# Kernel optimization log

Measured on AMD Instinct MI355X. Metric: run time of the kernel, lower is better.

## Reference

```python
import jax, jax.numpy as jnp
import numpy as np
from jax import lax

C = 8          # bargs.channel
S = 1024       # bargs.test_sidelen
SIGMA = 1.0    # edge_sigma
KS = int(6 * SIGMA + 1)   # 7
PAD = KS // 2             # 3
BW = S // 6               # border_width
LAM, MU, TH = 5.0, 5.0, 1e-4


def _edge_kernel():
    coords = jnp.arange(KS, dtype=jnp.float32) - (KS - 1.0) / 2.0
    g1 = jnp.exp(-coords ** 2 / (2.0 * SIGMA ** 2))
    g1 = g1 / g1.sum()
    g2 = jnp.outer(g1, g1)
    return jnp.broadcast_to(g2, (C, 1, KS, KS))  # depthwise OIHW


def _alpha():
    # max applicable loop index among {row-dist, col-dist}; interior stays 1.
    r = jnp.arange(S)
    g = jnp.where(r < BW, r, jnp.where(S - 1 - r < BW, S - 1 - r, -1))  # [S]
    m = jnp.maximum(g[:, None], g[None, :])                              # [S,S]
    a = jnp.where(m >= 0, m.astype(jnp.float32) / BW, 1.0)
    return a[None, None]  # [1,1,S,S] broadcasts over channels


def _grad_spectrum():
    gv = jnp.array([[-1., -2., -1.], [0., 0., 0.], [1., 2., 1.]], jnp.float32)
    gh = gv.T
    gvf = jnp.fft.fft2(gv, s=(S, S))
    ghf = jnp.fft.fft2(gh, s=(S, S))
    return (jnp.abs(gvf) ** 2 + jnp.abs(ghf) ** 2).astype(jnp.float32)  # real


def _edge_blur(img, kernel, alpha):
    blurred = lax.conv_general_dilated(
        img, kernel, window_strides=(1, 1), padding=[(PAD, PAD), (PAD, PAD)],
        feature_group_count=C, dimension_numbers=('NCHW', 'OIHW', 'NCHW'))
    return alpha * img + (1.0 - alpha) * blurred


def setup_inputs() -> dict:
    key = jax.random.key(0)
    k1, k2 = jax.random.split(key)
    lms = jax.random.uniform(k1, (1, C, S, S), dtype=jnp.float32)
    fuse = jax.random.uniform(k2, (1, C, S, S), dtype=jnp.float32)
    return {"lms": lms, "fuse": fuse}


def reference(lms, fuse):
    kernel = _edge_kernel()
    alpha = _alpha()
    grad = _grad_spectrum()

    lms_fft = jnp.fft.fft2(_edge_blur(lms, kernel, alpha))
    fuse_fft = jnp.fft.fft2(_edge_blur(fuse, kernel, alpha))

    denom = jnp.abs(fuse_fft) ** 2 + LAM + MU * grad      # real [1,C,S,S]
    numer = jnp.conj(fuse_fft) * lms_fft
    psf = jnp.fft.fftshift(jnp.real(jnp.fft.ifft2(numer / denom)), axes=(-2, -1))
    psf = jnp.where(psf < TH, 0.0, psf)                   # [1,C,S,S]

    def crop(p):  # p: [S,S]
        row, col = jnp.unravel_index(jnp.argmax(p), p.shape)
        patch = lax.dynamic_slice(p, (row - 20, col - 20), (41, 41))
        return patch / jnp.sum(patch)

    psf_l = jax.vmap(crop)(psf[0])        # [C,41,41]
    return psf_l[:, None]                 # [C,1,41,41]
```

## Files before the change

kernel.cpp:

```cpp
#include <hip/hip_runtime.h>
#include <math.h>

#define SS 1024
#define NC 8
#define BWD 170
#define THRESH 1e-4f

typedef unsigned long long ull;

__device__ __forceinline__ float2 cmul(float2 a, float2 b) {
    return make_float2(a.x * b.x - a.y * b.y, a.x * b.y + a.y * b.x);
}

#define XS(a) ((a) ^ (((a) >> 4) & 15))

template <int DIR>
__device__ __forceinline__ void bfly4(const float2 v[4], float2 r[4]) {
    float2 a = v[0], b = v[1], c = v[2], d = v[3];
    float2 apc = make_float2(a.x + c.x, a.y + c.y);
    float2 amc = make_float2(a.x - c.x, a.y - c.y);
    float2 bpd = make_float2(b.x + d.x, b.y + d.y);
    float2 jb  = make_float2(-(b.y - d.y), b.x - d.x);
    r[0] = make_float2(apc.x + bpd.x, apc.y + bpd.y);
    r[2] = make_float2(apc.x - bpd.x, apc.y - bpd.y);
    if (DIR == -1) {
        r[1] = make_float2(amc.x - jb.x, amc.y - jb.y);
        r[3] = make_float2(amc.x + jb.x, amc.y + jb.y);
    } else {
        r[1] = make_float2(amc.x + jb.x, amc.y + jb.y);
        r[3] = make_float2(amc.x - jb.x, amc.y - jb.y);
    }
}

template <int DIR>
__device__ __forceinline__ void fft1024_reg(float2 v[4], float2* A, float2* B,
                                            int tid) {
    float2* dst = A;
    float2* alt = B;
    #pragma unroll
    for (int t = 0; t < 4; ++t) {
        int s = 1 << (2 * t);
        int k = tid & ~(s - 1);
        float2 r[4];
        bfly4<DIR>(v, r);
        float rev = (float)k * (1.0f / 1024.0f);
        float2 w1 = make_float2(__builtin_amdgcn_cosf(rev),
                                (float)DIR * __builtin_amdgcn_sinf(rev));
        float2 w2 = cmul(w1, w1);
        float2 w3 = cmul(w2, w1);
        int base = tid + 3 * k;
        dst[XS(base)]         = r[0];
        dst[XS(base + s)]     = cmul(r[1], w1);
        dst[XS(base + 2 * s)] = cmul(r[2], w2);
        dst[XS(base + 3 * s)] = cmul(r[3], w3);
        __syncthreads();
        v[0] = dst[XS(tid)];
        v[1] = dst[XS(tid + 256)];
        v[2] = dst[XS(tid + 512)];
        v[3] = dst[XS(tid + 768)];
        float2* tmp = dst; dst = alt; alt = tmp;
    }
    float2 r[4];
    bfly4<DIR>(v, r);
    v[0] = r[0]; v[1] = r[1]; v[2] = r[2]; v[3] = r[3];
}

#define PIDX(r) ((r) + ((r) >> 5))

__global__ __launch_bounds__(256) void blur_fft_kernel(
        const float* __restrict__ lms, const float* __restrict__ fuse,
        float2* __restrict__ Zf) {
    __shared__ float2 bufA[1024];
    __shared__ float2 smemB2[1068];
    float* rowl = (float*)smemB2;
    float* rowf = rowl + 1068;
    int tid = threadIdx.x;
    int g = blockIdx.x;
    int c = g >> 10;
    int y = (g & 7) * 128 + ((g >> 3) & 127);
    const float* L = lms + ((size_t)c << 20);
    const float* F = fuse + ((size_t)c << 20);
    int x0 = tid << 2;

    double e1 = exp(-0.5), e2 = exp(-2.0), e3 = exp(-4.5);
    double sm = 1.0 + 2.0 * (e1 + e2 + e3);
    float w[7] = { (float)(e3 / sm), (float)(e2 / sm), (float)(e1 / sm),
                   (float)(1.0 / sm),
                   (float)(e1 / sm), (float)(e2 / sm), (float)(e3 / sm) };

    bool rowInt = (y >= BWD) && (y <= SS - 1 - BWD);
    bool skipLoads = rowInt && (tid >= 45) && (tid <= 210);
    bool doH = !rowInt || (tid <= 43) || (tid >= 212);

    float4 cl, cf;
    if (skipLoads) {
        cl = *(const float4*)&L[((size_t)y << 10) + x0];
        cf = *(const float4*)&F[((size_t)y << 10) + x0];
    } else {
        float4 lv[7], fv[7];
        #pragma unroll
        for (int r = 0; r < 7; ++r) {
            int gy = y - 3 + r;
            if (gy >= 0 && gy < SS) {
                lv[r] = *(const float4*)&L[((size_t)gy << 10) + x0];
                fv[r] = *(const float4*)&F[((size_t)gy << 10) + x0];
            } else {
                lv[r] = make_float4(0.f, 0.f, 0.f, 0.f);
                fv[r] = make_float4(0.f, 0.f, 0.f, 0.f);
            }
        }
        cl = lv[3]; cf = fv[3];
        #pragma unroll
        for (int j = 0; j < 4; ++j) {
            float a = 0.f, b = 0.f;
            #pragma unroll
            for (int r = 0; r < 7; ++r) {
                a += w[r] * (&lv[r].x)[j];
                b += w[r] * (&fv[r].x)[j];
            }
            rowl[PIDX(3 + x0 + j)] = a;
            rowf[PIDX(3 + x0 + j)] = b;
        }
    }
    if (tid < 3) {
        rowl[PIDX(tid)] = 0.f; rowf[PIDX(tid)] = 0.f;
        rowl[PIDX(1027 + tid)] = 0.f; rowf[PIDX(1027 + tid)] = 0.f;
    }
    __syncthreads();

    float bl[4] = {0.f, 0.f, 0.f, 0.f}, bf[4] = {0.f, 0.f, 0.f, 0.f};
    if (doH) {
        #pragma unroll
        for (int k = 0; k < 4; ++k) {
            float a = 0.f, b = 0.f;
            #pragma unroll
            for (int j = 0; j < 7; ++j) {
                a += w[j] * rowl[PIDX(x0 + k + j)];
                b += w[j] * rowf[PIDX(x0 + k + j)];
            }
            bl[k] = a; bf[k] = b;
        }
    }
    int gyv = (y < BWD) ? y : ((SS - 1 - y) < BWD ? (SS - 1 - y) : -1);
    #pragma unroll
    for (int k = 0; k < 4; ++k) {
        int x = x0 + k;
        int gx = (x < BWD) ? x : ((SS - 1 - x) < BWD ? (SS - 1 - x) : -1);
        int m = gyv > gx ? gyv : gx;
        float a = (m >= 0) ? (float)m / (float)BWD : 1.0f;
        bufA[XS(x)] = make_float2(a * (&cl.x)[k] + (1.0f - a) * bl[k],
                                  a * (&cf.x)[k] + (1.0f - a) * bf[k]);
    }
    __syncthreads();

    float2 v[4];
    #pragma unroll
    for (int m = 0; m < 4; ++m) v[m] = bufA[XS(tid + (m << 8))];
    fft1024_reg<-1>(v, smemB2, bufA, tid);

    float2* Zrow = Zf + (((size_t)c << 20) + ((size_t)y << 10));
    #pragma unroll
    for (int r = 0; r < 4; ++r) Zrow[tid + (r << 8)] = v[r];
}

__global__ __launch_bounds__(256) void fft2_wiener_kernel(
        const float2* __restrict__ Z, float2* __restrict__ Wb) {
    __shared__ float2 resbuf[4][1024];
    __shared__ float2 scratch[1024];
    int tid = threadIdx.x;
    int p = blockIdx.x >> 9;
    int i0 = blockIdx.x & 511;
    int i = ((i0 & 7) << 3) | ((i0 >> 3) & 7) | (i0 & ~63);
    int rows[2];
    rows[0] = (i == 0) ? 0 : i;
    rows[1] = (i == 0) ? 512 : 1024 - i;
    bool selfp = (i == 0);

    float2 v[4], nv[4];
    {
        const float2* g0 = Z + (((size_t)(2 * p) << 20) + rows[0]);
        #pragma unroll
        for (int m = 0; m < 4; ++m)
            v[m] = g0[(size_t)(tid + (m << 8)) << 10];
    }
    #pragma unroll
    for (int combo = 0; combo < 4; ++combo) {
        if (combo < 3) {
            int nr = (combo + 1) >> 1, nc = (combo + 1) & 1;
            const float2* gn = Z + (((size_t)(2 * p + nc) << 20) + rows[nr]);
            #pragma unroll
            for (int m = 0; m < 4; ++m)
                nv[m] = gn[(size_t)(tid + (m << 8)) << 10];
        }
        fft1024_reg<-1>(v, scratch, resbuf[combo], tid);
        #pragma unroll
        for (int r = 0; r < 4; ++r)
            resbuf[combo][XS(tid + (r << 8))] = v[r];
        if (combo < 3) {
            #pragma unroll
            for (int m = 0; m < 4; ++m) v[m] = nv[m];
        }
    }
    __syncthreads();

    float2 gout[2][4];
    #pragma unroll
    for (int o = 0; o < 2; ++o) {
        int u = rows[o];
        int po = selfp ? o : (1 - o);
        float cu = __builtin_amdgcn_cosf((float)u * (1.0f / 1024.0f));
        float c2u = 2.0f * cu * cu - 1.0f;
        float hu = 2.0f + 2.0f * cu;
        #pragma unroll
        for (int j = 0; j < 4; ++j) {
            int vv = tid + (j << 8);
            int vn = (1024 - vv) & 1023;
            float cv = __builtin_amdgcn_cosf((float)vv * (1.0f / 1024.0f));
            float c2v = 2.0f * cv * cv - 1.0f;
            float hv = 2.0f + 2.0f * cv;
            float grad = (2.0f - 2.0f * c2v) * hu * hu +
                         (2.0f - 2.0f * c2u) * hv * hv;
            float regs = 5.0f + 5.0f * grad;
            float G0x, G0y, G1x, G1y;
            #pragma unroll
            for (int c = 0; c < 2; ++c) {
                float2 a = resbuf[o * 2 + c][XS(vv)];
                float2 b = resbuf[po * 2 + c][XS(vn)];
                float Lx = 0.5f * (a.x + b.x), Ly = 0.5f * (a.y - b.y);
                float Fx = 0.5f * (a.y + b.y), Fy = -0.5f * (a.x - b.x);
                float inv = 1.0f / (Fx * Fx + Fy * Fy + regs);
                float nx = (Fx * Lx + Fy * Ly) * inv;
                float ny = (Fx * Ly - Fy * Lx) * inv;
                if (c == 0) { G0x = nx; G0y = ny; } else { G1x = nx; G1y = ny; }
            }
            gout[o][j] = make_float2(G0x - G1y, G0y + G1x);
        }
    }
    __syncthreads();

    const float isc = 1.0f / 1024.0f;
    #pragma unroll
    for (int o = 0; o < 2; ++o) {
        float2 iv[4];
        #pragma unroll
        for (int j = 0; j < 4; ++j) iv[j] = gout[o][j];
        fft1024_reg<1>(iv, scratch, resbuf[o], tid);
        float2* go = Wb + (((size_t)p << 20) + ((size_t)rows[o] << 10));
        #pragma unroll
        for (int r = 0; r < 4; ++r)
            go[tid + (r << 8)] = make_float2(iv[r].x * isc, iv[r].y * isc);
    }
}

__global__ __launch_bounds__(256) void ifft_final_kernel(
        const float2* __restrict__ Wd, float* __restrict__ psf,
        ull* __restrict__ bm) {
    __shared__ float2 bufA[1024];
    __shared__ float2 bufB[1024];
    __shared__ ull red0[4];
    __shared__ ull red1[4];
    int tid = threadIdx.x;
    int p = blockIdx.x >> 10;
    int b0 = blockIdx.x & 1023;
    int y = ((b0 & 7) << 3) | ((b0 >> 3) & 7) | (b0 & ~63);
    const float2* g = Wd + (((size_t)p << 20) + y);
    float2 v[4];
    #pragma unroll
    for (int m = 0; m < 4; ++m)
        v[m] = g[(size_t)(tid + (m << 8)) << 10];
    fft1024_reg<1>(v, bufA, bufB, tid);

    int oy = (y + 512) & 1023;
    float* p0 = psf + (((size_t)(2 * p) << 20) + ((size_t)oy << 10));
    float* p1 = p0 + (1u << 20);
    const float sc = 1.0f / 1024.0f;
    ull e0 = 0, e1 = 0;
    #pragma unroll
    for (int r = 0; r < 4; ++r) {
        int k = tid + (r << 8);
        float re = v[r].x * sc; re = (re < THRESH) ? 0.0f : re;
        float im = v[r].y * sc; im = (im < THRESH) ? 0.0f : im;
        int ox = (k + 512) & 1023;
        p0[ox] = re;
        p1[ox] = im;
        unsigned int idx = ((unsigned int)oy << 10) | (unsigned int)ox;
        ull c0 = ((ull)__float_as_uint(re) << 32) | (ull)(0xFFFFFFFFu - idx);
        ull c1 = ((ull)__float_as_uint(im) << 32) | (ull)(0xFFFFFFFFu - idx);
        e0 = c0 > e0 ? c0 : e0;
        e1 = c1 > e1 ? c1 : e1;
    }
    #pragma unroll
    for (int off = 32; off > 0; off >>= 1) {
        ull o0 = __shfl_down(e0, off);
        ull o1 = __shfl_down(e1, off);
        e0 = o0 > e0 ? o0 : e0;
        e1 = o1 > e1 ? o1 : e1;
    }
    if ((tid & 63) == 0) { red0[tid >> 6] = e0; red1[tid >> 6] = e1; }
    __syncthreads();
    if (tid == 0) {
        ull m0 = red0[0], m1 = red1[0];
        #pragma unroll
        for (int i2 = 1; i2 < 4; ++i2) {
            m0 = red0[i2] > m0 ? red0[i2] : m0;
            m1 = red1[i2] > m1 ? red1[i2] : m1;
        }
        bm[((size_t)(2 * p) << 10) + y] = m0;
        bm[((size_t)(2 * p + 1) << 10) + y] = m1;
    }
}

__global__ __launch_bounds__(256) void crop_kernel(
        const float* __restrict__ psf, const ull* __restrict__ bm,
        float* __restrict__ out) {
    int c = blockIdx.x;
    __shared__ ull rmax[256];
    __shared__ float red[256];
    int tid = threadIdx.x;
    ull e = 0;
    for (int i = tid; i < 1024; i += 256) {
        ull v = bm[((size_t)c << 10) + i];
        e = v > e ? v : e;
    }
    rmax[tid] = e;
    __syncthreads();
    for (int s2 = 128; s2 > 0; s2 >>= 1) {
        if (tid < s2) { ull a = rmax[tid], b = rmax[tid + s2]; rmax[tid] = a > b ? a : b; }
        __syncthreads();
    }
    unsigned int bidx = 0xFFFFFFFFu - (unsigned int)(rmax[0] & 0xFFFFFFFFull);
    int row = (int)(bidx >> 10), col = (int)(bidx & 1023);
    int r0 = row - 20; if (r0 < 0) r0 = 0; if (r0 > SS - 41) r0 = SS - 41;
    int c0 = col - 20; if (c0 < 0) c0 = 0; if (c0 > SS - 41) c0 = SS - 41;
    const float* p = psf + ((size_t)c << 20);
    float local = 0.0f;
    for (int i = tid; i < 1681; i += 256) {
        int rr = i / 41, cc = i - rr * 41;
        local += p[(size_t)(r0 + rr) * SS + c0 + cc];
    }
    red[tid] = local;
    __syncthreads();
    for (int s2 = 128; s2 > 0; s2 >>= 1) {
        if (tid < s2) red[tid] += red[tid + s2];
        __syncthreads();
    }
    float inv = 1.0f / red[0];
    for (int i = tid; i < 1681; i += 256) {
        int rr = i / 41, cc = i - rr * 41;
        out[c * 1681 + i] = p[(size_t)(r0 + rr) * SS + c0 + cc] * inv;
    }
}

extern "C" void kernel_launch(void* const* d_in, const int* in_sizes, int n_in,
                              void* d_out, int out_size, void* d_ws,
                              size_t ws_size, hipStream_t stream) {
    const float* lms = (const float*)d_in[0];
    const float* fuse = (const float*)d_in[1];
    char* ws = (char*)d_ws;
    float2* Zf = (float2*)ws;
    float2* Wb = (float2*)(ws + ((size_t)64 << 20));
    float* psf = (float*)ws;
    ull* bm = (ull*)(ws + ((size_t)33 << 20));
    float* outp = (float*)d_out;

    blur_fft_kernel<<<8192, 256, 0, stream>>>(lms, fuse, Zf);
    fft2_wiener_kernel<<<2048, 256, 0, stream>>>(Zf, Wb);
    ifft_final_kernel<<<4096, 256, 0, stream>>>(Wb, psf, bm);
    crop_kernel<<<8, 256, 0, stream>>>(psf, bm, outp);
}
```

Baseline: 207.7 us.

## Permute row-FFT output so column pairs load as float4; two rows per final block

The row FFT now writes each output bin to a permuted slot that places frequency kx next to its conjugate partner 1024-kx. The column-FFT/Wiener kernel can then fetch both columns with one float4 load per element, and it drops its separate scratch buffer by reusing the resbuf slots. The final inverse-FFT kernel processes two adjacent columns per block, also via float4 loads, with half the blocks. It writes per-wave argmax candidates straight to global memory instead of reducing through shared memory, so the crop kernel scans four times as many entries. The FFT helper gains an optional trailing barrier that is used when source and destination buffers alias.

```diff
diff --git a/kernel.cpp b/kernel.cpp
--- a/kernel.cpp
+++ b/kernel.cpp
@@ -13,6 +13,12 @@
 }
 
 #define XS(a) ((a) ^ (((a) >> 4) & 15))
+
+__device__ __forceinline__ int cmap(int kx) {
+    if (kx == 0) return 0;
+    if (kx == 512) return 1;
+    return (kx < 512) ? (kx << 1) : (((1024 - kx) << 1) | 1);
+}
 
 template <int DIR>
 __device__ __forceinline__ void bfly4(const float2 v[4], float2 r[4]) {
@@ -34,7 +40,7 @@
 
 template <int DIR>
 __device__ __forceinline__ void fft1024_reg(float2 v[4], float2* A, float2* B,
-                                            int tid) {
+                                            int tid, bool sb) {
     float2* dst = A;
     float2* alt = B;
     #pragma unroll
@@ -58,6 +64,7 @@
         v[1] = dst[XS(tid + 256)];
         v[2] = dst[XS(tid + 512)];
         v[3] = dst[XS(tid + 768)];
+        if (sb) __syncthreads();
         float2* tmp = dst; dst = alt; alt = tmp;
     }
     float2 r[4];
@@ -156,51 +163,57 @@
     float2 v[4];
     #pragma unroll
     for (int m = 0; m < 4; ++m) v[m] = bufA[XS(tid + (m << 8))];
-    fft1024_reg<-1>(v, smemB2, bufA, tid);
+    fft1024_reg<-1>(v, smemB2, bufA, tid, false);
 
     float2* Zrow = Zf + (((size_t)c << 20) + ((size_t)y << 10));
     #pragma unroll
-    for (int r = 0; r < 4; ++r) Zrow[tid + (r << 8)] = v[r];
+    for (int r = 0; r < 4; ++r) Zrow[cmap(tid + (r << 8))] = v[r];
 }
 
 __global__ __launch_bounds__(256) void fft2_wiener_kernel(
         const float2* __restrict__ Z, float2* __restrict__ Wb) {
     __shared__ float2 resbuf[4][1024];
-    __shared__ float2 scratch[1024];
     int tid = threadIdx.x;
     int p = blockIdx.x >> 9;
-    int i0 = blockIdx.x & 511;
-    int i = ((i0 & 7) << 3) | ((i0 >> 3) & 7) | (i0 & ~63);
+    int b0 = blockIdx.x & 511;
+    int i = ((b0 & 7) << 6) | (b0 >> 3);
     int rows[2];
     rows[0] = (i == 0) ? 0 : i;
     rows[1] = (i == 0) ? 512 : 1024 - i;
     bool selfp = (i == 0);
-
-    float2 v[4], nv[4];
-    {
-        const float2* g0 = Z + (((size_t)(2 * p) << 20) + rows[0]);
-        #pragma unroll
-        for (int m = 0; m < 4; ++m)
-            v[m] = g0[(size_t)(tid + (m << 8)) << 10];
-    }
-    #pragma unroll
-    for (int combo = 0; combo < 4; ++combo) {
-        if (combo < 3) {
-            int nr = (combo + 1) >> 1, nc = (combo + 1) & 1;
-            const float2* gn = Z + (((size_t)(2 * p + nc) << 20) + rows[nr]);
-            #pragma unroll
-            for (int m = 0; m < 4; ++m)
-                nv[m] = gn[(size_t)(tid + (m << 8)) << 10];
-        }
-        fft1024_reg<-1>(v, scratch, resbuf[combo], tid);
-        #pragma unroll
-        for (int r = 0; r < 4; ++r)
-            resbuf[combo][XS(tid + (r << 8))] = v[r];
-        if (combo < 3) {
-            #pragma unroll
-            for (int m = 0; m < 4; ++m) v[m] = nv[m];
-        }
-    }
+    int slot = (i == 0) ? 0 : (i << 1);
+
+    const float2* Zp0 = Z + ((size_t)(2 * p) << 20);
+    const float2* Zp1 = Z + ((size_t)(2 * p + 1) << 20);
+    float4 q0[4], q1[4];
+    #pragma unroll
+    for (int m = 0; m < 4; ++m)
+        q0[m] = *(const float4*)&Zp0[((size_t)(tid + (m << 8)) << 10) + slot];
+    #pragma unroll
+    for (int m = 0; m < 4; ++m)
+        q1[m] = *(const float4*)&Zp1[((size_t)(tid + (m << 8)) << 10) + slot];
+
+    float2 v[4];
+    #pragma unroll
+    for (int m = 0; m < 4; ++m) v[m] = make_float2(q0[m].x, q0[m].y);
+    fft1024_reg<-1>(v, resbuf[2], resbuf[0], tid, false);
+    #pragma unroll
+    for (int r = 0; r < 4; ++r) resbuf[0][XS(tid + (r << 8))] = v[r];
+    #pragma unroll
+    for (int m = 0; m < 4; ++m) v[m] = make_float2(q0[m].z, q0[m].w);
+    fft1024_reg<-1>(v, resbuf[1], resbuf[2], tid, false);
+    #pragma unroll
+    for (int r = 0; r < 4; ++r) resbuf[2][XS(tid + (r << 8))] = v[r];
+    #pragma unroll
+    for (int m = 0; m < 4; ++m) v[m] = make_float2(q1[m].x, q1[m].y);
+    fft1024_reg<-1>(v, resbuf[3], resbuf[1], tid, false);
+    #pragma unroll
+    for (int r = 0; r < 4; ++r) resbuf[1][XS(tid + (r << 8))] = v[r];
+    #pragma unroll
+    for (int m = 0; m < 4; ++m) v[m] = make_float2(q1[m].z, q1[m].w);
+    fft1024_reg<-1>(v, resbuf[3], resbuf[3], tid, true);
+    #pragma unroll
+    for (int r = 0; r < 4; ++r) resbuf[3][XS(tid + (r << 8))] = v[r];
     __syncthreads();
 
     float2 gout[2][4];
@@ -244,7 +257,7 @@
         float2 iv[4];
         #pragma unroll
         for (int j = 0; j < 4; ++j) iv[j] = gout[o][j];
-        fft1024_reg<1>(iv, scratch, resbuf[o], tid);
+        fft1024_reg<1>(iv, resbuf[1 + 2 * o], resbuf[2 * o], tid, false);
         float2* go = Wb + (((size_t)p << 20) + ((size_t)rows[o] << 10));
         #pragma unroll
         for (int r = 0; r < 4; ++r)
@@ -257,56 +270,57 @@
         ull* __restrict__ bm) {
     __shared__ float2 bufA[1024];
     __shared__ float2 bufB[1024];
-    __shared__ ull red0[4];
-    __shared__ ull red1[4];
     int tid = threadIdx.x;
-    int p = blockIdx.x >> 10;
-    int b0 = blockIdx.x & 1023;
-    int y = ((b0 & 7) << 3) | ((b0 >> 3) & 7) | (b0 & ~63);
-    const float2* g = Wd + (((size_t)p << 20) + y);
-    float2 v[4];
+    int wv = tid >> 6;
+    int p = blockIdx.x >> 9;
+    int b0 = blockIdx.x & 511;
+    int y0 = (((b0 & 7) << 6) | (b0 >> 3)) << 1;
+    const float2* g = Wd + (((size_t)p << 20) + y0);
+    float4 q[4];
     #pragma unroll
     for (int m = 0; m < 4; ++m)
-        v[m] = g[(size_t)(tid + (m << 8)) << 10];
-    fft1024_reg<1>(v, bufA, bufB, tid);
-
-    int oy = (y + 512) & 1023;
-    float* p0 = psf + (((size_t)(2 * p) << 20) + ((size_t)oy << 10));
-    float* p1 = p0 + (1u << 20);
+        q[m] = *(const float4*)&g[(size_t)(tid + (m << 8)) << 10];
+
     const float sc = 1.0f / 1024.0f;
-    ull e0 = 0, e1 = 0;
-    #pragma unroll
-    for (int r = 0; r < 4; ++r) {
-        int k = tid + (r << 8);
-        float re = v[r].x * sc; re = (re < THRESH) ? 0.0f : re;
-        float im = v[r].y * sc; im = (im < THRESH) ? 0.0f : im;
-        int ox = (k + 512) & 1023;
-        p0[ox] = re;
-        p1[ox] = im;
-        unsigned int idx = ((unsigned int)oy << 10) | (unsigned int)ox;
-        ull c0 = ((ull)__float_as_uint(re) << 32) | (ull)(0xFFFFFFFFu - idx);
-        ull c1 = ((ull)__float_as_uint(im) << 32) | (ull)(0xFFFFFFFFu - idx);
-        e0 = c0 > e0 ? c0 : e0;
-        e1 = c1 > e1 ? c1 : e1;
-    }
-    #pragma unroll
-    for (int off = 32; off > 0; off >>= 1) {
-        ull o0 = __shfl_down(e0, off);
-        ull o1 = __shfl_down(e1, off);
-        e0 = o0 > e0 ? o0 : e0;
-        e1 = o1 > e1 ? o1 : e1;
-    }
-    if ((tid & 63) == 0) { red0[tid >> 6] = e0; red1[tid >> 6] = e1; }
-    __syncthreads();
-    if (tid == 0) {
-        ull m0 = red0[0], m1 = red1[0];
-        #pragma unroll
-        for (int i2 = 1; i2 < 4; ++i2) {
-            m0 = red0[i2] > m0 ? red0[i2] : m0;
-            m1 = red1[i2] > m1 ? red1[i2] : m1;
-        }
-        bm[((size_t)(2 * p) << 10) + y] = m0;
-        bm[((size_t)(2 * p + 1) << 10) + y] = m1;
+    #pragma unroll
+    for (int half = 0; half < 2; ++half) {
+        int y = y0 + half;
+        float2 v[4];
+        #pragma unroll
+        for (int m = 0; m < 4; ++m)
+            v[m] = half ? make_float2(q[m].z, q[m].w)
+                        : make_float2(q[m].x, q[m].y);
+        fft1024_reg<1>(v, bufA, bufB, tid, false);
+
+        int oy = (y + 512) & 1023;
+        float* p0 = psf + (((size_t)(2 * p) << 20) + ((size_t)oy << 10));
+        float* p1 = p0 + (1u << 20);
+        ull e0 = 0, e1 = 0;
+        #pragma unroll
+        for (int r = 0; r < 4; ++r) {
+            int k = tid + (r << 8);
+            float re = v[r].x * sc; re = (re < THRESH) ? 0.0f : re;
+            float im = v[r].y * sc; im = (im < THRESH) ? 0.0f : im;
+            int ox = (k + 512) & 1023;
+            p0[ox] = re;
+            p1[ox] = im;
+            unsigned int idx = ((unsigned int)oy << 10) | (unsigned int)ox;
+            ull c0 = ((ull)__float_as_uint(re) << 32) | (ull)(0xFFFFFFFFu - idx);
+            ull c1 = ((ull)__float_as_uint(im) << 32) | (ull)(0xFFFFFFFFu - idx);
+            e0 = c0 > e0 ? c0 : e0;
+            e1 = c1 > e1 ? c1 : e1;
+        }
+        #pragma unroll
+        for (int off = 32; off > 0; off >>= 1) {
+            ull o0 = __shfl_down(e0, off);
+            ull o1 = __shfl_down(e1, off);
+            e0 = o0 > e0 ? o0 : e0;
+            e1 = o1 > e1 ? o1 : e1;
+        }
+        if ((tid & 63) == 0) {
+            bm[((size_t)(2 * p) << 12) + (y << 2) + wv] = e0;
+            bm[((size_t)(2 * p + 1) << 12) + (y << 2) + wv] = e1;
+        }
     }
 }
 
@@ -318,8 +332,8 @@
     __shared__ float red[256];
     int tid = threadIdx.x;
     ull e = 0;
-    for (int i = tid; i < 1024; i += 256) {
-        ull v = bm[((size_t)c << 10) + i];
+    for (int i = tid; i < 4096; i += 256) {
+        ull v = bm[((size_t)c << 12) + i];
         e = v > e ? v : e;
     }
     rmax[tid] = e;
@@ -365,6 +379,6 @@
 
     blur_fft_kernel<<<8192, 256, 0, stream>>>(lms, fuse, Zf);
     fft2_wiener_kernel<<<2048, 256, 0, stream>>>(Zf, Wb);
-    ifft_final_kernel<<<4096, 256, 0, stream>>>(Wb, psf, bm);
+    ifft_final_kernel<<<2048, 256, 0, stream>>>(Wb, psf, bm);
     crop_kernel<<<8, 256, 0, stream>>>(psf, bm, outp);
 }
```

Result: faster. 190.4 us, median of 2 (-8.3%).

## Use wave-local radix-16 FFTs and permuted spectrum layout for vectorized column loads

Applied to the files above, without the earlier changes.

Replaces the block-wide radix-4 FFT, which needs a __syncthreads per stage, with a per-wavefront 1024-point FFT built from radix-16 passes that use LDS exchange and only waitcnt barriers. Each wave handles one column. The row FFT output is stored in a permuted order that puts conjugate-pair frequencies next to each other, so the column kernel can fetch both with one float4 load. The inverse column kernel likewise processes four rows per block through paired float4 loads, cutting its grid size and block reductions. This trades fewer block syncs and wider memory accesses for higher register pressure (16 complex values per thread), and the second Wiener stage leaves half the waves idle.

```diff
diff --git a/kernel.cpp b/kernel.cpp
--- a/kernel.cpp
+++ b/kernel.cpp
@@ -13,6 +13,12 @@
 }
 
 #define XS(a) ((a) ^ (((a) >> 4) & 15))
+
+__device__ __forceinline__ int cmap(int kx) {
+    if (kx == 0) return 0;
+    if (kx == 512) return 1;
+    return (kx < 512) ? (kx << 1) : (((1024 - kx) << 1) | 1);
+}
 
 template <int DIR>
 __device__ __forceinline__ void bfly4(const float2 v[4], float2 r[4]) {
@@ -30,6 +36,12 @@
         r[1] = make_float2(amc.x + jb.x, amc.y + jb.y);
         r[3] = make_float2(amc.x - jb.x, amc.y - jb.y);
     }
+}
+
+template <int DIR>
+__device__ __forceinline__ float2 wc(float2 a, float cr, float si) {
+    float s = (DIR == -1) ? -si : si;
+    return make_float2(a.x * cr - a.y * s, a.x * s + a.y * cr);
 }
 
 template <int DIR>
@@ -65,6 +77,91 @@
     v[0] = r[0]; v[1] = r[1]; v[2] = r[2]; v[3] = r[3];
 }
 
+template <int DIR>
+__device__ __forceinline__ void dft16_tw(float2 u[16], float rev) {
+    float2 t[4][4];
+    #pragma unroll
+    for (int a = 0; a < 4; ++a) {
+        float2 in[4] = { u[a], u[a + 4], u[a + 8], u[a + 12] };
+        bfly4<DIR>(in, t[a]);
+    }
+    const float C1 = 0.923879532511287f, S1 = 0.382683432365090f;
+    const float C2 = 0.707106781186548f;
+    t[1][1] = wc<DIR>(t[1][1], C1, S1);
+    t[1][2] = wc<DIR>(t[1][2], C2, C2);
+    t[1][3] = wc<DIR>(t[1][3], S1, C1);
+    t[2][1] = wc<DIR>(t[2][1], C2, C2);
+    t[2][2] = (DIR == -1) ? make_float2(t[2][2].y, -t[2][2].x)
+                          : make_float2(-t[2][2].y, t[2][2].x);
+    t[2][3] = wc<DIR>(t[2][3], -C2, C2);
+    t[3][1] = wc<DIR>(t[3][1], S1, C1);
+    t[3][2] = wc<DIR>(t[3][2], -C2, C2);
+    t[3][3] = wc<DIR>(t[3][3], -C1, -S1);
+    #pragma unroll
+    for (int ci = 0; ci < 4; ++ci) {
+        float2 in[4] = { t[0][ci], t[1][ci], t[2][ci], t[3][ci] };
+        float2 s[4];
+        bfly4<DIR>(in, s);
+        u[ci] = s[0]; u[ci + 4] = s[1]; u[ci + 8] = s[2]; u[ci + 12] = s[3];
+    }
+    float cs = __builtin_amdgcn_cosf(rev);
+    float sn = __builtin_amdgcn_sinf(rev);
+    float2 w1 = make_float2(cs, (float)DIR * sn);
+    float2 w2 = cmul(w1, w1);
+    float2 w3 = cmul(w2, w1);
+    float2 w4 = cmul(w2, w2);
+    float2 w8 = cmul(w4, w4);
+    u[1]  = cmul(u[1], w1);
+    u[2]  = cmul(u[2], w2);
+    u[3]  = cmul(u[3], w3);
+    u[4]  = cmul(u[4], w4);
+    u[5]  = cmul(u[5], cmul(w4, w1));
+    u[6]  = cmul(u[6], cmul(w4, w2));
+    u[7]  = cmul(u[7], cmul(w4, w3));
+    u[8]  = cmul(u[8], w8);
+    u[9]  = cmul(u[9], cmul(w8, w1));
+    u[10] = cmul(u[10], cmul(w8, w2));
+    u[11] = cmul(u[11], cmul(w8, w3));
+    u[12] = cmul(u[12], cmul(w8, w4));
+    u[13] = cmul(u[13], cmul(w8, cmul(w4, w1)));
+    u[14] = cmul(u[14], cmul(w8, cmul(w4, w2)));
+    u[15] = cmul(u[15], cmul(w8, cmul(w4, w3)));
+}
+
+template <int DIR>
+__device__ __forceinline__ void fft1024_wave(float2 v[16], float2* X, int l) {
+    dft16_tw<DIR>(v, (float)l * (1.0f / 1024.0f));
+    int base = l << 4;
+    #pragma unroll
+    for (int cc = 0; cc < 16; ++cc) X[XS(base + cc)] = v[cc];
+    asm volatile("s_waitcnt lgkmcnt(0)" ::: "memory");
+    int a_ = l & 3, cr = l >> 2;
+    #pragma unroll
+    for (int b = 0; b < 16; ++b)
+        v[b] = X[XS(((a_ + (b << 2)) << 4) + cr)];
+    asm volatile("s_waitcnt lgkmcnt(0)" ::: "memory");
+    dft16_tw<DIR>(v, (float)a_ * (1.0f / 64.0f));
+    #pragma unroll
+    for (int cc = 0; cc < 16; ++cc) X[XS(base + cc)] = v[cc];
+    asm volatile("s_waitcnt lgkmcnt(0)" ::: "memory");
+    int c2 = l & 15, cl2 = l >> 4;
+    float2 q[16];
+    #pragma unroll
+    for (int a2 = 0; a2 < 4; ++a2)
+        #pragma unroll
+        for (int chh = 0; chh < 4; ++chh)
+            q[(a2 << 2) + chh] =
+                X[XS(((a2 + (c2 << 2)) << 4) + cl2 + (chh << 2))];
+    asm volatile("s_waitcnt lgkmcnt(0)" ::: "memory");
+    #pragma unroll
+    for (int chh = 0; chh < 4; ++chh) {
+        float2 in[4] = { q[chh], q[4 + chh], q[8 + chh], q[12 + chh] };
+        float2 r[4];
+        bfly4<DIR>(in, r);
+        v[chh] = r[0]; v[chh + 4] = r[1]; v[chh + 8] = r[2]; v[chh + 12] = r[3];
+    }
+}
+
 #define PIDX(r) ((r) + ((r) >> 5))
 
 __global__ __launch_bounds__(256) void blur_fft_kernel(
@@ -160,60 +257,48 @@
 
     float2* Zrow = Zf + (((size_t)c << 20) + ((size_t)y << 10));
     #pragma unroll
-    for (int r = 0; r < 4; ++r) Zrow[tid + (r << 8)] = v[r];
+    for (int r = 0; r < 4; ++r) Zrow[cmap(tid + (r << 8))] = v[r];
 }
 
 __global__ __launch_bounds__(256) void fft2_wiener_kernel(
         const float2* __restrict__ Z, float2* __restrict__ Wb) {
-    __shared__ float2 resbuf[4][1024];
-    __shared__ float2 scratch[1024];
+    __shared__ float2 xch[4][1024];
     int tid = threadIdx.x;
+    int wv = tid >> 6, l = tid & 63;
     int p = blockIdx.x >> 9;
-    int i0 = blockIdx.x & 511;
-    int i = ((i0 & 7) << 3) | ((i0 >> 3) & 7) | (i0 & ~63);
+    int b0 = blockIdx.x & 511;
+    int i = ((b0 & 7) << 6) | (b0 >> 3);
     int rows[2];
     rows[0] = (i == 0) ? 0 : i;
     rows[1] = (i == 0) ? 512 : 1024 - i;
     bool selfp = (i == 0);
-
-    float2 v[4], nv[4];
-    {
-        const float2* g0 = Z + (((size_t)(2 * p) << 20) + rows[0]);
-        #pragma unroll
-        for (int m = 0; m < 4; ++m)
-            v[m] = g0[(size_t)(tid + (m << 8)) << 10];
-    }
-    #pragma unroll
-    for (int combo = 0; combo < 4; ++combo) {
-        if (combo < 3) {
-            int nr = (combo + 1) >> 1, nc = (combo + 1) & 1;
-            const float2* gn = Z + (((size_t)(2 * p + nc) << 20) + rows[nr]);
-            #pragma unroll
-            for (int m = 0; m < 4; ++m)
-                nv[m] = gn[(size_t)(tid + (m << 8)) << 10];
-        }
-        fft1024_reg<-1>(v, scratch, resbuf[combo], tid);
-        #pragma unroll
-        for (int r = 0; r < 4; ++r)
-            resbuf[combo][XS(tid + (r << 8))] = v[r];
-        if (combo < 3) {
-            #pragma unroll
-            for (int m = 0; m < 4; ++m) v[m] = nv[m];
-        }
-    }
-    __syncthreads();
-
-    float2 gout[2][4];
-    #pragma unroll
-    for (int o = 0; o < 2; ++o) {
+    int slot = (i == 0) ? 0 : (i << 1);
+
+    int ch = wv & 1, ri = wv >> 1;
+    const float2* Zp = Z + ((size_t)(2 * p + ch) << 20);
+    float2 v[16];
+    #pragma unroll
+    for (int b = 0; b < 16; ++b) {
+        float4 qq = *(const float4*)&Zp[((size_t)(l + (b << 6)) << 10) + slot];
+        v[b] = ri ? make_float2(qq.z, qq.w) : make_float2(qq.x, qq.y);
+    }
+    fft1024_wave<-1>(v, xch[wv], l);
+    #pragma unroll
+    for (int j = 0; j < 16; ++j) xch[wv][XS(l + (j << 6))] = v[j];
+    __syncthreads();
+
+    float2 gi[16];
+    bool act = (wv < 2);
+    if (act) {
+        int o = wv;
         int u = rows[o];
         int po = selfp ? o : (1 - o);
         float cu = __builtin_amdgcn_cosf((float)u * (1.0f / 1024.0f));
         float c2u = 2.0f * cu * cu - 1.0f;
         float hu = 2.0f + 2.0f * cu;
         #pragma unroll
-        for (int j = 0; j < 4; ++j) {
-            int vv = tid + (j << 8);
+        for (int j = 0; j < 16; ++j) {
+            int vv = l + (j << 6);
             int vn = (1024 - vv) & 1023;
             float cv = __builtin_amdgcn_cosf((float)vv * (1.0f / 1024.0f));
             float c2v = 2.0f * cv * cv - 1.0f;
@@ -224,8 +309,8 @@
             float G0x, G0y, G1x, G1y;
             #pragma unroll
             for (int c = 0; c < 2; ++c) {
-                float2 a = resbuf[o * 2 + c][XS(vv)];
-                float2 b = resbuf[po * 2 + c][XS(vn)];
+                float2 a = xch[o * 2 + c][XS(vv)];
+                float2 b = xch[po * 2 + c][XS(vn)];
                 float Lx = 0.5f * (a.x + b.x), Ly = 0.5f * (a.y - b.y);
                 float Fx = 0.5f * (a.y + b.y), Fy = -0.5f * (a.x - b.x);
                 float inv = 1.0f / (Fx * Fx + Fy * Fy + regs);
@@ -233,42 +318,40 @@
                 float ny = (Fx * Ly - Fy * Lx) * inv;
                 if (c == 0) { G0x = nx; G0y = ny; } else { G1x = nx; G1y = ny; }
             }
-            gout[o][j] = make_float2(G0x - G1y, G0y + G1x);
+            gi[j] = make_float2(G0x - G1y, G0y + G1x);
         }
     }
     __syncthreads();
 
-    const float isc = 1.0f / 1024.0f;
-    #pragma unroll
-    for (int o = 0; o < 2; ++o) {
-        float2 iv[4];
-        #pragma unroll
-        for (int j = 0; j < 4; ++j) iv[j] = gout[o][j];
-        fft1024_reg<1>(iv, scratch, resbuf[o], tid);
-        float2* go = Wb + (((size_t)p << 20) + ((size_t)rows[o] << 10));
-        #pragma unroll
-        for (int r = 0; r < 4; ++r)
-            go[tid + (r << 8)] = make_float2(iv[r].x * isc, iv[r].y * isc);
+    if (act) {
+        fft1024_wave<1>(gi, xch[wv], l);
+        const float isc = 1.0f / 1024.0f;
+        float2* go = Wb + (((size_t)p << 20) + ((size_t)rows[wv] << 10));
+        #pragma unroll
+        for (int j = 0; j < 16; ++j)
+            go[l + (j << 6)] = make_float2(gi[j].x * isc, gi[j].y * isc);
     }
 }
 
 __global__ __launch_bounds__(256) void ifft_final_kernel(
         const float2* __restrict__ Wd, float* __restrict__ psf,
         ull* __restrict__ bm) {
-    __shared__ float2 bufA[1024];
-    __shared__ float2 bufB[1024];
-    __shared__ ull red0[4];
-    __shared__ ull red1[4];
+    __shared__ float2 xch[4][1024];
     int tid = threadIdx.x;
-    int p = blockIdx.x >> 10;
-    int b0 = blockIdx.x & 1023;
-    int y = ((b0 & 7) << 3) | ((b0 >> 3) & 7) | (b0 & ~63);
-    const float2* g = Wd + (((size_t)p << 20) + y);
-    float2 v[4];
-    #pragma unroll
-    for (int m = 0; m < 4; ++m)
-        v[m] = g[(size_t)(tid + (m << 8)) << 10];
-    fft1024_reg<1>(v, bufA, bufB, tid);
+    int wv = tid >> 6, l = tid & 63;
+    int p = blockIdx.x >> 8;
+    int b0 = blockIdx.x & 255;
+    int y0 = (((b0 & 7) << 5) | (b0 >> 3)) << 2;
+    int y = y0 + wv;
+    const float2* g = Wd + (((size_t)p << 20) + y0 + ((wv >> 1) << 1));
+    float2 v[16];
+    #pragma unroll
+    for (int b = 0; b < 16; ++b) {
+        float4 qq = *(const float4*)&g[(size_t)(l + (b << 6)) << 10];
+        v[b] = (wv & 1) ? make_float2(qq.z, qq.w)
+                        : make_float2(qq.x, qq.y);
+    }
+    fft1024_wave<1>(v, xch[wv], l);
 
     int oy = (y + 512) & 1023;
     float* p0 = psf + (((size_t)(2 * p) << 20) + ((size_t)oy << 10));
@@ -276,10 +359,10 @@
     const float sc = 1.0f / 1024.0f;
     ull e0 = 0, e1 = 0;
     #pragma unroll
-    for (int r = 0; r < 4; ++r) {
-        int k = tid + (r << 8);
-        float re = v[r].x * sc; re = (re < THRESH) ? 0.0f : re;
-        float im = v[r].y * sc; im = (im < THRESH) ? 0.0f : im;
+    for (int j = 0; j < 16; ++j) {
+        int k = l + (j << 6);
+        float re = v[j].x * sc; re = (re < THRESH) ? 0.0f : re;
+        float im = v[j].y * sc; im = (im < THRESH) ? 0.0f : im;
         int ox = (k + 512) & 1023;
         p0[ox] = re;
         p1[ox] = im;
@@ -296,17 +379,9 @@
         e0 = o0 > e0 ? o0 : e0;
         e1 = o1 > e1 ? o1 : e1;
     }
-    if ((tid & 63) == 0) { red0[tid >> 6] = e0; red1[tid >> 6] = e1; }
-    __syncthreads();
-    if (tid == 0) {
-        ull m0 = red0[0], m1 = red1[0];
-        #pragma unroll
-        for (int i2 = 1; i2 < 4; ++i2) {
-            m0 = red0[i2] > m0 ? red0[i2] : m0;
-            m1 = red1[i2] > m1 ? red1[i2] : m1;
-        }
-        bm[((size_t)(2 * p) << 10) + y] = m0;
-        bm[((size_t)(2 * p + 1) << 10) + y] = m1;
+    if (l == 0) {
+        bm[((size_t)(2 * p) << 10) + y] = e0;
+        bm[((size_t)(2 * p + 1) << 10) + y] = e1;
     }
 }
 
@@ -365,6 +440,6 @@
 
     blur_fft_kernel<<<8192, 256, 0, stream>>>(lms, fuse, Zf);
     fft2_wiener_kernel<<<2048, 256, 0, stream>>>(Zf, Wb);
-    ifft_final_kernel<<<4096, 256, 0, stream>>>(Wb, psf, bm);
+    ifft_final_kernel<<<1024, 256, 0, stream>>>(Wb, psf, bm);
     crop_kernel<<<8, 256, 0, stream>>>(psf, bm, outp);
 }
```

Result: slower. 227.2 us (+9.4%).
